# Kernel tuning notes

Measured on AMD Instinct MI355X. Metric: run time of the kernel, lower is better.

The kernel has to match this reference:

```python
import jax, jax.numpy as jnp
import numpy as np

B, CIN, COUT, H, W, REP = 8, 512, 64, 28, 28, 1024


def setup_inputs() -> dict:
    key = jax.random.key(0)
    ks = jax.random.split(key, 7)
    scale_conv = 1.0 / np.sqrt(CIN * 9)
    scale_fc6 = 1.0 / np.sqrt(CIN * COUT)
    scale_fc7 = 1.0 / np.sqrt(REP)
    return {
        "x": jax.random.normal(ks[0], (B, CIN, H, W), jnp.float32),
        "conv_w": jax.random.normal(ks[1], (COUT, CIN, 3, 3), jnp.float32) * scale_conv,
        "conv_b": jax.random.normal(ks[2], (COUT,), jnp.float32) * scale_conv,
        "fc6_w": jax.random.normal(ks[3], (REP, CIN * COUT), jnp.float32) * scale_fc6,
        "fc6_b": jax.random.normal(ks[4], (REP,), jnp.float32) * scale_fc6,
        "fc7_w": jax.random.normal(ks[5], (REP, REP), jnp.float32) * scale_fc7,
        "fc7_b": jax.random.normal(ks[6], (REP,), jnp.float32) * scale_fc7,
    }


def reference(x, conv_w, conv_b, fc6_w, fc6_b, fc7_w, fc7_b):
    # attention_map: (B, COUT, H, W) -- 3x3 conv, stride 1, pad 1 ('SAME')
    am = jax.lax.conv_general_dilated(
        x, conv_w, window_strides=(1, 1), padding="SAME",
        dimension_numbers=("NCHW", "OIHW", "NCHW"),
    ) + conv_b[None, :, None, None]
    # outer product (B, CIN, COUT, H, W) then global max-pool over H, W
    outer = am[:, None, :, :, :] * x[:, :, None, :, :]
    x_pool = jnp.max(outer, axis=(3, 4))  # (B, CIN, COUT)
    # eval-mode path: pooled features -> fc6 -> relu -> fc7 -> relu
    flat = x_pool.reshape(x.shape[0], -1)  # (B, CIN*COUT)
    h = jax.nn.relu(flat @ fc6_w.T + fc6_b)
    out = jax.nn.relu(h @ fc7_w.T + fc7_b)
    return (out, x_pool)
```

## Files before the change

### kernel.cpp

```cpp
#include <hip/hip_runtime.h>

typedef __attribute__((ext_vector_type(4))) float f32x4;
typedef __attribute__((ext_vector_type(8))) __bf16 bf16x8;
typedef __attribute__((ext_vector_type(8))) unsigned short ushort8;
typedef __attribute__((ext_vector_type(4))) unsigned short u16x4;

static __device__ __forceinline__ unsigned short f2bf(float f) {
  unsigned u = __float_as_uint(f);
  u += 0x7fffu + ((u >> 16) & 1u);
  return (unsigned short)(u >> 16);
}
static __device__ __forceinline__ float bf2f(unsigned short s) {
  return __uint_as_float(((unsigned)s) << 16);
}

__global__ __launch_bounds__(256, 1) void k_xpose(
    const float* __restrict__ x, const float* __restrict__ cw,
    unsigned short* __restrict__ xT, unsigned short* __restrict__ wpk) {
  int bid = blockIdx.x;
  int t = threadIdx.x;
  if (bid < 896) {
    __shared__ float xl[64 * 57];
    int pt = bid % 14, cit = (bid / 14) & 7, b = bid / 112;
    int p0 = pt * 56, ci0 = cit * 64;
#pragma unroll
    for (int i = 0; i < 4; ++i) {
      int idx = i * 256 + t;
      if (idx < 896) {
        int ci = idx / 14, p4 = (idx % 14) * 4;
        f32x4 v = *reinterpret_cast<const f32x4*>(
            x + ((size_t)(b * 512 + ci0 + ci)) * 784 + p0 + p4);
        *reinterpret_cast<f32x4*>(&xl[ci * 57 + p4]) = v;
      }
    }
    __syncthreads();
#pragma unroll
    for (int i = 0; i < 2; ++i) {
      int idx = i * 256 + t;
      if (idx < 448) {
        int p = idx >> 3, c8 = (idx & 7) * 8;
        ushort8 o;
#pragma unroll
        for (int j = 0; j < 8; ++j) o[j] = f2bf(xl[(c8 + j) * 57 + p]);
        *reinterpret_cast<ushort8*>(
            xT + ((size_t)(b * 784 + p0 + p)) * 512 + ci0 + c8) = o;
      }
    }
  } else {
    int o0 = (bid - 896) * 4096 + t * 16;
    ushort8 w0, w1;
#pragma unroll
    for (int j = 0; j < 16; ++j) {
      int o = o0 + j;
      int ci = o & 511, co = (o >> 9) & 63, tap = o >> 15;
      unsigned short v = f2bf(cw[((size_t)(co * 512 + ci)) * 9 + tap]);
      if (j < 8) w0[j] = v; else w1[j - 8] = v;
    }
    *reinterpret_cast<ushort8*>(wpk + o0) = w0;
    *reinterpret_cast<ushort8*>(wpk + o0 + 8) = w1;
  }
}

#define CPAD 56
__global__ __launch_bounds__(128, 1) void k_conv(
    const unsigned short* __restrict__ xT, const unsigned short* __restrict__ wpk,
    const float* __restrict__ cb, float* __restrict__ am_part) {
  __shared__ unsigned short wl[9 * 32 * CPAD];
  __shared__ unsigned short xl[168 * CPAD];
  int bid = blockIdx.x;
  int s  = bid & 3;
  int c2 = (bid >> 2) & 1;
  int px = (bid >> 3) % 7;
  int b  = bid / 56;
  int t = threadIdx.x;
  int W = t >> 6, lane = t & 63;
  int co_base = c2 * 32;
  int p0 = px * 112, h0 = px * 4;
  int n = lane & 15, kg = lane >> 4;

  int lrow0[7], wc[7];
#pragma unroll
  for (int f = 0; f < 7; ++f) {
    int pit = f * 16 + n;
    lrow0[f] = pit / 28 + 1;
    wc[f]    = pit % 28;
  }
  f32x4 acc[7];
  f32x4 cb4 = {0.f, 0.f, 0.f, 0.f};
  if (s == 0)
    cb4 = *reinterpret_cast<const f32x4*>(cb + co_base + W * 16 + kg * 4);
#pragma unroll
  for (int f = 0; f < 7; ++f) acc[f] = cb4;
  const ushort8 bzero = {0, 0, 0, 0, 0, 0, 0, 0};

  for (int c = 0; c < 4; ++c) {
    int ci_c = s * 128 + c * 32;
    __syncthreads();
#pragma unroll
    for (int i = 0; i < 9; ++i) {
      int q = i * 128 + t;
      int tapco = q >> 2, ci8 = (q & 3) * 8;
      int tap = tapco >> 5, co_l = tapco & 31;
      ushort8 v = *reinterpret_cast<const ushort8*>(
          wpk + ((size_t)(tap * 64 + co_base + co_l)) * 512 + ci_c + ci8);
      *reinterpret_cast<ushort8*>(&wl[(tap * 32 + co_l) * CPAD + ci8]) = v;
    }
#pragma unroll
    for (int i = 0; i < 6; ++i) {
      int q = i * 128 + t;
      if (q < 672) {
        int pos = q >> 2, ci8 = (q & 3) * 8;
        int lr = pos / 28, c_ = pos % 28;
        int h = h0 - 1 + lr;
        ushort8 v = bzero;
        if (h >= 0 && h < 28)
          v = *reinterpret_cast<const ushort8*>(
              xT + ((size_t)(b * 784 + h * 28 + c_)) * 512 + ci_c + ci8);
        *reinterpret_cast<ushort8*>(&xl[pos * CPAD + ci8]) = v;
      }
    }
    __syncthreads();
#pragma unroll
    for (int tap = 0; tap < 9; ++tap) {
      int dh = tap / 3 - 1, dw = tap % 3 - 1;
      bf16x8 a = *reinterpret_cast<const bf16x8*>(
          &wl[(tap * 32 + W * 16 + n) * CPAD + kg * 8]);
#pragma unroll
      for (int f = 0; f < 7; ++f) {
        int wcd = wc[f] + dw;
        bool valid = (unsigned)wcd < 28u;
        int pos = (lrow0[f] + dh) * 28 + wcd;
        int posc = valid ? pos : 0;
        ushort8 bv = *reinterpret_cast<const ushort8*>(&xl[posc * CPAD + kg * 8]);
        if (!valid) bv = bzero;
        acc[f] = __builtin_amdgcn_mfma_f32_16x16x32_bf16(
            a, __builtin_bit_cast(bf16x8, bv), acc[f], 0, 0, 0);
      }
    }
  }
#pragma unroll
  for (int f = 0; f < 7; ++f) {
    int p  = p0 + f * 16 + n;
    int co = co_base + W * 16 + kg * 4;
    *reinterpret_cast<f32x4*>(
        am_part + ((size_t)((s * 8 + b) * 784 + p)) * 64 + co) = acc[f];
  }
}

#define XP2 72
#define AP2 72
__global__ __launch_bounds__(256, 1) void k_pool(
    const unsigned short* __restrict__ xT, const float* __restrict__ am_part,
    float* __restrict__ pmax) {
  __shared__ unsigned short xls[112 * XP2];
  __shared__ float aml[112 * AP2];
  int bid = blockIdx.x;
  int pc  = bid % 7;
  int cit = (bid / 7) & 7;
  int b   = bid / 56;
  int t = threadIdx.x;
  int p0 = pc * 112, ci0 = cit * 64;
#pragma unroll
  for (int i = 0; i < 4; ++i) {
    int idx = i * 256 + t;
    if (idx < 896) {
      int p = idx >> 3, c8 = (idx & 7) * 8;
      ushort8 v = *reinterpret_cast<const ushort8*>(
          xT + ((size_t)(b * 784 + p0 + p)) * 512 + ci0 + c8);
      *reinterpret_cast<ushort8*>(&xls[p * XP2 + c8]) = v;
    }
  }
#pragma unroll
  for (int i = 0; i < 7; ++i) {
    int idx = i * 256 + t;
    int p = idx >> 4, co4 = (idx & 15) * 4;
    size_t o0 = ((size_t)(b * 784 + p0 + p)) * 64 + co4;
    f32x4 v = *reinterpret_cast<const f32x4*>(am_part + o0);
#pragma unroll
    for (int s2 = 1; s2 < 4; ++s2)
      v = v + *reinterpret_cast<const f32x4*>(am_part + o0 + (size_t)s2 * 8 * 784 * 64);
    *reinterpret_cast<f32x4*>(&aml[p * AP2 + co4]) = v;
  }
  __syncthreads();
  int half = t >> 7;
  int t1 = t & 127;
  int cig = t1 >> 3;
  int cog = t1 & 7;
  int pb = half * 56;
  float m[4][8];
#pragma unroll
  for (int i = 0; i < 4; ++i)
#pragma unroll
    for (int j = 0; j < 8; ++j) m[i][j] = -3.4e38f;
  for (int pp = 0; pp < 56; pp += 2) {
    int p = pb + pp;
    u16x4 xs0 = *reinterpret_cast<const u16x4*>(&xls[p * XP2 + cig * 4]);
    u16x4 xs1 = *reinterpret_cast<const u16x4*>(&xls[(p + 1) * XP2 + cig * 4]);
    f32x4 a00 = *reinterpret_cast<const f32x4*>(&aml[p * AP2 + cog * 8]);
    f32x4 a01 = *reinterpret_cast<const f32x4*>(&aml[p * AP2 + cog * 8 + 4]);
    f32x4 a10 = *reinterpret_cast<const f32x4*>(&aml[(p + 1) * AP2 + cog * 8]);
    f32x4 a11 = *reinterpret_cast<const f32x4*>(&aml[(p + 1) * AP2 + cog * 8 + 4]);
    float xv0[4], xv1[4], av0[8], av1[8];
#pragma unroll
    for (int i = 0; i < 4; ++i) { xv0[i] = bf2f(xs0[i]); xv1[i] = bf2f(xs1[i]); }
#pragma unroll
    for (int j = 0; j < 4; ++j) {
      av0[j] = a00[j]; av0[j + 4] = a01[j];
      av1[j] = a10[j]; av1[j + 4] = a11[j];
    }
#pragma unroll
    for (int i = 0; i < 4; ++i)
#pragma unroll
      for (int j = 0; j < 8; ++j)
        m[i][j] = fmaxf(fmaxf(m[i][j], xv0[i] * av0[j]), xv1[i] * av1[j]);
  }
  int pcc = pc * 2 + half;
#pragma unroll
  for (int i = 0; i < 4; ++i) {
    f32x4 v0 = {m[i][0], m[i][1], m[i][2], m[i][3]};
    f32x4 v1 = {m[i][4], m[i][5], m[i][6], m[i][7]};
    size_t o = ((size_t)((pcc * 8 + b) * 512 + ci0 + cig * 4 + i)) * 64 + cog * 8;
    *reinterpret_cast<f32x4*>(pmax + o) = v0;
    *reinterpret_cast<f32x4*>(pmax + o + 4) = v1;
  }
}

__global__ __launch_bounds__(256, 1) void k_combine(
    const float* __restrict__ pmax, float* __restrict__ xpool) {
  size_t idx = ((size_t)blockIdx.x * 256 + threadIdx.x) * 4;
  f32x4 v = *reinterpret_cast<const f32x4*>(pmax + idx);
#pragma unroll
  for (int pcc = 1; pcc < 14; ++pcc) {
    f32x4 u = *reinterpret_cast<const f32x4*>(pmax + (size_t)pcc * 262144 + idx);
#pragma unroll
    for (int j = 0; j < 4; ++j) v[j] = fmaxf(v[j], u[j]);
  }
  *reinterpret_cast<f32x4*>(xpool + idx) = v;
}

__global__ __launch_bounds__(256) void k_fc6(
    const float* __restrict__ flat, const float* __restrict__ w6,
    float* __restrict__ part6) {
  __shared__ float red[4][8][33];
  int bid = blockIdx.x;
  int kc = bid & 7, rg = bid >> 3;
  int t = threadIdx.x, W = t >> 6, lane = t & 63;
  int r0 = rg * 4;
  int kbase = kc * 4096 + t * 4;
  const float* fp = flat + kbase;
  const float* wp = w6 + (size_t)r0 * 32768 + kbase;
  float acc[4][8];
#pragma unroll
  for (int r = 0; r < 4; ++r)
#pragma unroll
    for (int b = 0; b < 8; ++b) acc[r][b] = 0.f;

  f32x4 fA[8], wA[4], fB[8], wB[4];
#define LOAD_SET(F, Wt, off)                                                   \
  {                                                                            \
    _Pragma("unroll")                                                          \
    for (int b = 0; b < 8; ++b)                                                \
      F[b] = *reinterpret_cast<const f32x4*>(fp + (size_t)b * 32768 + (off));  \
    _Pragma("unroll")                                                          \
    for (int r = 0; r < 4; ++r)                                                \
      Wt[r] = *reinterpret_cast<const f32x4*>(wp + (size_t)r * 32768 + (off)); \
  }
#define COMP_SET(F, Wt)                                                        \
  {                                                                            \
    _Pragma("unroll")                                                          \
    for (int r = 0; r < 4; ++r)                                                \
      _Pragma("unroll")                                                        \
      for (int b = 0; b < 8; ++b)                                              \
        acc[r][b] += Wt[r][0] * F[b][0] + Wt[r][1] * F[b][1] +                 \
                     Wt[r][2] * F[b][2] + Wt[r][3] * F[b][3];                  \
  }
  LOAD_SET(fA, wA, 0)
  LOAD_SET(fB, wB, 1024)
  COMP_SET(fA, wA)
  LOAD_SET(fA, wA, 2048)
  COMP_SET(fB, wB)
  LOAD_SET(fB, wB, 3072)
  COMP_SET(fA, wA)
  COMP_SET(fB, wB)
#undef LOAD_SET
#undef COMP_SET

#pragma unroll
  for (int r = 0; r < 4; ++r)
#pragma unroll
    for (int b = 0; b < 8; ++b) {
      float v = acc[r][b];
      v += __shfl_down(v, 32, 64);
      v += __shfl_down(v, 16, 64);
      v += __shfl_down(v, 8, 64);
      acc[r][b] = v;
    }
  if (lane < 8) {
#pragma unroll
    for (int r = 0; r < 4; ++r)
#pragma unroll
      for (int b = 0; b < 8; ++b) red[W][lane][r * 8 + b] = acc[r][b];
  }
  __syncthreads();
  if (t < 32) {
    float sum = 0.f;
#pragma unroll
    for (int w = 0; w < 4; ++w)
#pragma unroll
      for (int l = 0; l < 8; ++l) sum += red[w][l][t];
    int r = t >> 3, b = t & 7;
    part6[(size_t)kc * 8192 + (r0 + r) * 8 + b] = sum;
  }
}

__global__ __launch_bounds__(256, 1) void k_h(
    const float* __restrict__ part6, const float* __restrict__ b6,
    float* __restrict__ h) {
  int idx = blockIdx.x * 256 + threadIdx.x;
  int r = idx >> 3, b = idx & 7;
  float s = b6[r];
#pragma unroll
  for (int kc = 0; kc < 8; ++kc) s += part6[(size_t)kc * 8192 + r * 8 + b];
  h[b * 1024 + r] = fmaxf(s, 0.f);
}

__global__ __launch_bounds__(256, 1) void k_fc7(
    const float* __restrict__ h, const float* __restrict__ w7,
    const float* __restrict__ b7, float* __restrict__ out) {
  int bid = blockIdx.x;
  int t = threadIdx.x, W = t >> 6, lane = t & 63;
  int r = bid * 4 + W;
  float acc[8] = {0, 0, 0, 0, 0, 0, 0, 0};
#pragma unroll
  for (int step = 0; step < 4; ++step) {
    int k = step * 256 + lane * 4;
    f32x4 w4 = *reinterpret_cast<const f32x4*>(w7 + (size_t)r * 1024 + k);
#pragma unroll
    for (int b = 0; b < 8; ++b) {
      f32x4 h4 = *reinterpret_cast<const f32x4*>(h + b * 1024 + k);
      acc[b] += w4[0] * h4[0] + w4[1] * h4[1] + w4[2] * h4[2] + w4[3] * h4[3];
    }
  }
#pragma unroll
  for (int b = 0; b < 8; ++b) {
    float v = acc[b];
#pragma unroll
    for (int off = 32; off > 0; off >>= 1) v += __shfl_down(v, off, 64);
    acc[b] = v;
  }
  if (lane == 0) {
#pragma unroll
    for (int b = 0; b < 8; ++b) out[b * 1024 + r] = fmaxf(acc[b] + b7[r], 0.f);
  }
}

extern "C" void kernel_launch(void* const* d_in, const int* in_sizes, int n_in,
                              void* d_out, int out_size, void* d_ws, size_t ws_size,
                              hipStream_t stream) {
  const float* x  = (const float*)d_in[0];
  const float* cw = (const float*)d_in[1];
  const float* cb = (const float*)d_in[2];
  const float* w6 = (const float*)d_in[3];
  const float* b6 = (const float*)d_in[4];
  const float* w7 = (const float*)d_in[5];
  const float* b7 = (const float*)d_in[6];
  float* out   = (float*)d_out;
  float* xpool = out + 8192;

  char* ws = (char*)d_ws;
  unsigned short* xT  = (unsigned short*)(ws);
  unsigned short* wpk = (unsigned short*)(ws + 6422528);
  float* am_part      = (float*)(ws + 7012352);
  float* pmax         = (float*)(ws + 13434880);
  float* part6        = (float*)(ws + 28114944);
  float* hbuf         = (float*)(ws + 28377088);

  hipLaunchKernelGGL(k_xpose,   dim3(968),  dim3(256), 0, stream, x, cw, xT, wpk);
  hipLaunchKernelGGL(k_conv,    dim3(448),  dim3(128), 0, stream, xT, wpk, cb, am_part);
  hipLaunchKernelGGL(k_pool,    dim3(448),  dim3(256), 0, stream, xT, am_part, pmax);
  hipLaunchKernelGGL(k_combine, dim3(256),  dim3(256), 0, stream, pmax, xpool);
  hipLaunchKernelGGL(k_fc6,     dim3(2048), dim3(256), 0, stream, xpool, w6, part6);
  hipLaunchKernelGGL(k_h,       dim3(32),   dim3(256), 0, stream, part6, b6, hbuf);
  hipLaunchKernelGGL(k_fc7,     dim3(256),  dim3(256), 0, stream, hbuf, w7, b7, out);
}
```

Baseline: 82.61 us.

## Store conv partials in bf16 and split fc6 reduction into more blocks

The conv kernel now writes its split-K partial attention maps as bf16 instead of fp32, halving the intermediate traffic between conv and pool. The pool kernel reads and sums these as bf16. Separately, fc6 now uses four times as many blocks, each handling a 1024-wide K chunk with a single load set, and k_h sums 32 partials instead of 8. This targets bandwidth parallelism on the 128MB fc6 weight stream, at the cost of lower precision in the attention map and more partial-sum traffic.

```diff
diff --git a/kernel.cpp b/kernel.cpp
--- a/kernel.cpp
+++ b/kernel.cpp
@@ -64,7 +64,7 @@
 #define CPAD 56
 __global__ __launch_bounds__(128, 1) void k_conv(
     const unsigned short* __restrict__ xT, const unsigned short* __restrict__ wpk,
-    const float* __restrict__ cb, float* __restrict__ am_part) {
+    const float* __restrict__ cb, unsigned short* __restrict__ am_part) {
   __shared__ unsigned short wl[9 * 32 * CPAD];
   __shared__ unsigned short xl[168 * CPAD];
   int bid = blockIdx.x;
@@ -142,15 +142,18 @@
   for (int f = 0; f < 7; ++f) {
     int p  = p0 + f * 16 + n;
     int co = co_base + W * 16 + kg * 4;
-    *reinterpret_cast<f32x4*>(
-        am_part + ((size_t)((s * 8 + b) * 784 + p)) * 64 + co) = acc[f];
+    u16x4 o;
+#pragma unroll
+    for (int j = 0; j < 4; ++j) o[j] = f2bf(acc[f][j]);
+    *reinterpret_cast<u16x4*>(
+        am_part + ((size_t)((s * 8 + b) * 784 + p)) * 64 + co) = o;
   }
 }
 
 #define XP2 72
 #define AP2 72
 __global__ __launch_bounds__(256, 1) void k_pool(
-    const unsigned short* __restrict__ xT, const float* __restrict__ am_part,
+    const unsigned short* __restrict__ xT, const unsigned short* __restrict__ am_part,
     float* __restrict__ pmax) {
   __shared__ unsigned short xls[112 * XP2];
   __shared__ float aml[112 * AP2];
@@ -171,15 +174,26 @@
     }
   }
 #pragma unroll
-  for (int i = 0; i < 7; ++i) {
+  for (int i = 0; i < 4; ++i) {
     int idx = i * 256 + t;
-    int p = idx >> 4, co4 = (idx & 15) * 4;
-    size_t o0 = ((size_t)(b * 784 + p0 + p)) * 64 + co4;
-    f32x4 v = *reinterpret_cast<const f32x4*>(am_part + o0);
-#pragma unroll
-    for (int s2 = 1; s2 < 4; ++s2)
-      v = v + *reinterpret_cast<const f32x4*>(am_part + o0 + (size_t)s2 * 8 * 784 * 64);
-    *reinterpret_cast<f32x4*>(&aml[p * AP2 + co4]) = v;
+    if (idx < 896) {
+      int p = idx >> 3, co8 = (idx & 7) * 8;
+      size_t o0 = ((size_t)(b * 784 + p0 + p)) * 64 + co8;
+      float sv[8];
+#pragma unroll
+      for (int j = 0; j < 8; ++j) sv[j] = 0.f;
+#pragma unroll
+      for (int s2 = 0; s2 < 4; ++s2) {
+        ushort8 u = *reinterpret_cast<const ushort8*>(
+            am_part + o0 + (size_t)s2 * 8 * 784 * 64);
+#pragma unroll
+        for (int j = 0; j < 8; ++j) sv[j] += bf2f(u[j]);
+      }
+      f32x4 v0 = {sv[0], sv[1], sv[2], sv[3]};
+      f32x4 v1 = {sv[4], sv[5], sv[6], sv[7]};
+      *reinterpret_cast<f32x4*>(&aml[p * AP2 + co8]) = v0;
+      *reinterpret_cast<f32x4*>(&aml[p * AP2 + co8 + 4]) = v1;
+    }
   }
   __syncthreads();
   int half = t >> 7;
@@ -243,48 +257,24 @@
     float* __restrict__ part6) {
   __shared__ float red[4][8][33];
   int bid = blockIdx.x;
-  int kc = bid & 7, rg = bid >> 3;
+  int kc = bid & 31, rg = bid >> 5;
   int t = threadIdx.x, W = t >> 6, lane = t & 63;
   int r0 = rg * 4;
-  int kbase = kc * 4096 + t * 4;
-  const float* fp = flat + kbase;
-  const float* wp = w6 + (size_t)r0 * 32768 + kbase;
+  int k = kc * 1024 + t * 4;
+  f32x4 f4[8], w4[4];
+#pragma unroll
+  for (int b = 0; b < 8; ++b)
+    f4[b] = *reinterpret_cast<const f32x4*>(flat + (size_t)b * 32768 + k);
+#pragma unroll
+  for (int r = 0; r < 4; ++r)
+    w4[r] = *reinterpret_cast<const f32x4*>(w6 + (size_t)(r0 + r) * 32768 + k);
   float acc[4][8];
 #pragma unroll
   for (int r = 0; r < 4; ++r)
 #pragma unroll
-    for (int b = 0; b < 8; ++b) acc[r][b] = 0.f;
-
-  f32x4 fA[8], wA[4], fB[8], wB[4];
-#define LOAD_SET(F, Wt, off)                                                   \
-  {                                                                            \
-    _Pragma("unroll")                                                          \
-    for (int b = 0; b < 8; ++b)                                                \
-      F[b] = *reinterpret_cast<const f32x4*>(fp + (size_t)b * 32768 + (off));  \
-    _Pragma("unroll")                                                          \
-    for (int r = 0; r < 4; ++r)                                                \
-      Wt[r] = *reinterpret_cast<const f32x4*>(wp + (size_t)r * 32768 + (off)); \
-  }
-#define COMP_SET(F, Wt)                                                        \
-  {                                                                            \
-    _Pragma("unroll")                                                          \
-    for (int r = 0; r < 4; ++r)                                                \
-      _Pragma("unroll")                                                        \
-      for (int b = 0; b < 8; ++b)                                              \
-        acc[r][b] += Wt[r][0] * F[b][0] + Wt[r][1] * F[b][1] +                 \
-                     Wt[r][2] * F[b][2] + Wt[r][3] * F[b][3];                  \
-  }
-  LOAD_SET(fA, wA, 0)
-  LOAD_SET(fB, wB, 1024)
-  COMP_SET(fA, wA)
-  LOAD_SET(fA, wA, 2048)
-  COMP_SET(fB, wB)
-  LOAD_SET(fB, wB, 3072)
-  COMP_SET(fA, wA)
-  COMP_SET(fB, wB)
-#undef LOAD_SET
-#undef COMP_SET
-
+    for (int b = 0; b < 8; ++b)
+      acc[r][b] = w4[r][0] * f4[b][0] + w4[r][1] * f4[b][1] +
+                  w4[r][2] * f4[b][2] + w4[r][3] * f4[b][3];
 #pragma unroll
   for (int r = 0; r < 4; ++r)
 #pragma unroll
@@ -320,7 +310,7 @@
   int r = idx >> 3, b = idx & 7;
   float s = b6[r];
 #pragma unroll
-  for (int kc = 0; kc < 8; ++kc) s += part6[(size_t)kc * 8192 + r * 8 + b];
+  for (int kc = 0; kc < 32; ++kc) s += part6[(size_t)kc * 8192 + r * 8 + b];
   h[b * 1024 + r] = fmaxf(s, 0.f);
 }
 
@@ -368,18 +358,18 @@
   float* xpool = out + 8192;
 
   char* ws = (char*)d_ws;
-  unsigned short* xT  = (unsigned short*)(ws);
-  unsigned short* wpk = (unsigned short*)(ws + 6422528);
-  float* am_part      = (float*)(ws + 7012352);
-  float* pmax         = (float*)(ws + 13434880);
-  float* part6        = (float*)(ws + 28114944);
-  float* hbuf         = (float*)(ws + 28377088);
+  unsigned short* xT      = (unsigned short*)(ws);
+  unsigned short* wpk     = (unsigned short*)(ws + 6422528);
+  unsigned short* am_part = (unsigned short*)(ws + 7012352);
+  float* pmax             = (float*)(ws + 10223616);
+  float* part6            = (float*)(ws + 24903680);
+  float* hbuf             = (float*)(ws + 25952256);
 
   hipLaunchKernelGGL(k_xpose,   dim3(968),  dim3(256), 0, stream, x, cw, xT, wpk);
   hipLaunchKernelGGL(k_conv,    dim3(448),  dim3(128), 0, stream, xT, wpk, cb, am_part);
   hipLaunchKernelGGL(k_pool,    dim3(448),  dim3(256), 0, stream, xT, am_part, pmax);
   hipLaunchKernelGGL(k_combine, dim3(256),  dim3(256), 0, stream, pmax, xpool);
-  hipLaunchKernelGGL(k_fc6,     dim3(2048), dim3(256), 0, stream, xpool, w6, part6);
+  hipLaunchKernelGGL(k_fc6,     dim3(8192), dim3(256), 0, stream, xpool, w6, part6);
   hipLaunchKernelGGL(k_h,       dim3(32),   dim3(256), 0, stream, part6, b6, hbuf);
   hipLaunchKernelGGL(k_fc7,     dim3(256),  dim3(256), 0, stream, hbuf, w7, b7, out);
 }
```

After: 98.10 us. 18.8% more time.
